# Optimization experiments

Measured on AMD Instinct MI355X. Metric: run time of the kernel, lower is better.

The kernel has to match this reference:

```python
import jax, jax.numpy as jnp
import numpy as np

B, T, D, H, L, V = 8, 1024, 1024, 16, 4, 50257
HD = D // H
DF = 4 * D
EPS = 1e-5


def _layernorm(x, w, b):
    m = jnp.mean(x, axis=-1, keepdims=True)
    v = jnp.mean((x - m) ** 2, axis=-1, keepdims=True)
    return (x - m) * jax.lax.rsqrt(v + EPS) * w + b


def setup_inputs() -> dict:
    key = jax.random.key(0)
    ks = jax.random.split(key, 17)
    s = 0.02
    n = lambda k, shape: (jax.random.normal(k, shape) * s).astype(jnp.float32)
    return {
        "idx": jax.random.randint(ks[0], (B, T), 0, V),
        "tok_emb": n(ks[1], (V, D)),
        "pos_emb": n(ks[2], (T, D)),
        "wq": n(ks[3], (L, D, D)),
        "wk": n(ks[4], (L, D, D)),
        "wv": n(ks[5], (L, D, D)),
        "w_proj": n(ks[6], (L, D, D)),
        "b_proj": jnp.zeros((L, D), jnp.float32),
        "ln1_w": jnp.ones((L, D), jnp.float32),
        "ln1_b": jnp.zeros((L, D), jnp.float32),
        "ln2_w": jnp.ones((L, D), jnp.float32),
        "ln2_b": jnp.zeros((L, D), jnp.float32),
        "w1": n(ks[7], (L, D, DF)),
        "b1": jnp.zeros((L, DF), jnp.float32),
        "w2": n(ks[8], (L, DF, D)),
        "b2": jnp.zeros((L, D), jnp.float32),
    }


def reference(idx, tok_emb, pos_emb, wq, wk, wv, w_proj, b_proj,
              ln1_w, ln1_b, ln2_w, ln2_b, w1, b1, w2, b2):
    b, t = idx.shape
    x = tok_emb[idx] + pos_emb[:t]  # [B,T,D]
    causal_mask = jnp.tril(jnp.ones((t, t), dtype=bool))  # [T,T]
    # NOTE: original scales by full embedding dim C**-0.5, not head_size
    scale = jnp.asarray(D, x.dtype) ** -0.5
    for l in range(L):
        h = _layernorm(x, ln1_w[l], ln1_b[l])
        q = (h @ wq[l]).reshape(b, t, H, HD)
        k = (h @ wk[l]).reshape(b, t, H, HD)
        v = (h @ wv[l]).reshape(b, t, H, HD)
        scores = jnp.einsum('bthd,bshd->bhts', q, k) * scale  # [B,H,T,T]
        scores = jnp.where(causal_mask, scores, -jnp.inf)
        attn = jax.nn.softmax(scores, axis=-1)
        ctx = jnp.einsum('bhts,bshd->bthd', attn, v).reshape(b, t, D)
        x = x + (ctx @ w_proj[l] + b_proj[l])
        h2 = _layernorm(x, ln2_w[l], ln2_b[l])
        ff = jax.nn.relu(h2 @ w1[l] + b1[l]) @ w2[l] + b2[l]
        x = x + ff  # fRes = 1.0 (linear_residual=True)
    return x
```

## Files before the change

### kernel.cpp

```cpp
#include <hip/hip_runtime.h>
#include <hip/hip_bf16.h>
#include <stdint.h>

typedef __hip_bfloat16 bf16;
typedef __attribute__((ext_vector_type(8))) short short8;
typedef __attribute__((ext_vector_type(4))) float f32x4;
typedef __attribute__((ext_vector_type(2))) unsigned int uint32x2;

static constexpr int TB = 8;
static constexpr int TT = 1024;
static constexpr int TD = 1024;
static constexpr int TH = 16;
static constexpr int TL = 4;
static constexpr int TDF = 4096;
static constexpr int TM = TB * TT;
static constexpr int QS = 3072;

#if __has_builtin(__builtin_amdgcn_permlane16_swap) && __has_builtin(__builtin_amdgcn_permlane32_swap)
#define USE_PERMLANE 1
#else
#define USE_PERMLANE 0
#endif

#define GLOAD16(g, l) __builtin_amdgcn_global_load_lds( \
    (const __attribute__((address_space(1))) unsigned int*)(g), \
    (__attribute__((address_space(3))) unsigned int*)(l), 16, 0, 0)

__global__ __launch_bounds__(256) void k_embed(const int* __restrict__ idx,
        const float* __restrict__ tok, const float* __restrict__ pos,
        float* __restrict__ x) {
    int row = blockIdx.x;
    int t = row & (TT - 1);
    int token = idx[row];
    int c = threadIdx.x * 4;
    float4 tv = *(const float4*)(tok + (int64_t)token * TD + c);
    float4 pv = *(const float4*)(pos + (int64_t)t * TD + c);
    *(float4*)(x + (int64_t)row * TD + c) =
        make_float4(tv.x + pv.x, tv.y + pv.y, tv.z + pv.z, tv.w + pv.w);
}

__global__ __launch_bounds__(256) void k_ln(const float* __restrict__ x,
        const float* __restrict__ w, const float* __restrict__ b,
        bf16* __restrict__ out) {
    int row = blockIdx.x;
    int tid = threadIdx.x;
    const float* xr = x + (int64_t)row * TD;
    float4 v = *(const float4*)(xr + tid * 4);
    float s  = v.x + v.y + v.z + v.w;
    float s2 = v.x*v.x + v.y*v.y + v.z*v.z + v.w*v.w;
    #pragma unroll
    for (int off = 32; off; off >>= 1) { s += __shfl_xor(s, off); s2 += __shfl_xor(s2, off); }
    __shared__ float red[8];
    int wv_ = tid >> 6, ln_ = tid & 63;
    if (ln_ == 0) { red[wv_] = s; red[4 + wv_] = s2; }
    __syncthreads();
    s  = red[0] + red[1] + red[2] + red[3];
    s2 = red[4] + red[5] + red[6] + red[7];
    float mean = s * (1.f / TD);
    float var  = s2 * (1.f / TD) - mean * mean;
    float rstd = rsqrtf(var + 1e-5f);
    float4 wv4 = *(const float4*)(w + tid * 4);
    float4 bv4 = *(const float4*)(b + tid * 4);
    bf16 t4[4];
    t4[0] = __float2bfloat16((v.x - mean) * rstd * wv4.x + bv4.x);
    t4[1] = __float2bfloat16((v.y - mean) * rstd * wv4.y + bv4.y);
    t4[2] = __float2bfloat16((v.z - mean) * rstd * wv4.z + bv4.z);
    t4[3] = __float2bfloat16((v.w - mean) * rstd * wv4.w + bv4.w);
    *(uint2*)(out + (int64_t)row * TD + tid * 4) = *(uint2*)t4;
}

__global__ __launch_bounds__(256) void k_wt(
        const float* __restrict__ wq, const float* __restrict__ wk,
        const float* __restrict__ wv, const float* __restrict__ wp,
        const float* __restrict__ w1, const float* __restrict__ w2,
        bf16* __restrict__ qkvT, bf16* __restrict__ wpT,
        bf16* __restrict__ w1T, bf16* __restrict__ w2T) {
    __shared__ bf16 tile[64 * 74];
    const int id = blockIdx.x;
    const float* src; bf16* dst; int K, N, n0, k0;
    if (id < 768) {
        int w = id >> 8, r = id & 255;
        src = (w == 0) ? wq : ((w == 1) ? wk : wv);
        dst = qkvT + (int64_t)w * 1024 * 1024;
        K = 1024; N = 1024; n0 = (r & 15) * 64; k0 = (r >> 4) * 64;
    } else if (id < 1024) {
        int r = id - 768; src = wp; dst = wpT;
        K = 1024; N = 1024; n0 = (r & 15) * 64; k0 = (r >> 4) * 64;
    } else if (id < 2048) {
        int r = id - 1024; src = w1; dst = w1T;
        K = 1024; N = 4096; n0 = (r & 63) * 64; k0 = (r >> 6) * 64;
    } else {
        int r = id - 2048; src = w2; dst = w2T;
        K = 4096; N = 1024; n0 = (r & 15) * 64; k0 = (r >> 4) * 64;
    }
    const int tid = threadIdx.x;
    #pragma unroll
    for (int i = 0; i < 16; i++) {
        int q = i * 256 + tid;
        int r = q >> 6, c = q & 63;
        tile[r * 74 + c] = __float2bfloat16(src[(int64_t)(k0 + r) * N + n0 + c]);
    }
    __syncthreads();
    #pragma unroll
    for (int i = 0; i < 16; i++) {
        int q = i * 256 + tid;
        int nr = q >> 6, kc = q & 63;
        dst[(int64_t)(n0 + nr) * K + k0 + kc] = tile[kc * 74 + nr];
    }
}

template<int EPI>
__global__ __launch_bounds__(512, 2) void k_gemm256(const bf16* __restrict__ A,
        const bf16* __restrict__ BT, const float* __restrict__ bias,
        const float* __restrict__ resid,
        float* __restrict__ outF, bf16* __restrict__ outB,
        bf16* __restrict__ vtp, int M, int N, int K) {
    extern __shared__ __align__(16) char smem[];
    const int tid = threadIdx.x;
    const int lane = tid & 63, wave = tid >> 6;
    const int wm = wave >> 2, wn = wave & 3;
    const int lr = lane & 15, lk = lane >> 4;
    const int nb = gridDim.x;
    const int sb = (blockIdx.x & 7) * (nb >> 3) + (blockIdx.x >> 3);
    const int nbn = N >> 8;
    const int bm = sb / nbn, bn = sb % nbn;
    const int64_t aBase = (int64_t)bm * 256 * K;
    const int64_t bBase = (int64_t)bn * 256 * K;
    const int NT = K >> 6;

    const int tswz = tid ^ (((tid >> 5) & 1) << 1);
    const int row0 = tswz >> 3, s0 = tswz & 7;

#define STAGE256(tt) do { \
        char* Ad_ = smem + (((tt) & 1) << 15); \
        char* Bd_ = smem + 65536 + (((tt) & 1) << 15); \
        _Pragma("unroll") \
        for (int j = 0; j < 4; j++) { \
            const int rr_ = j * 64 + row0; \
            GLOAD16(A  + aBase + (int64_t)rr_ * K + (tt) * 64 + s0 * 8, Ad_ + (j * 512 + tid) * 16); \
            GLOAD16(BT + bBase + (int64_t)rr_ * K + (tt) * 64 + s0 * 8, Bd_ + (j * 512 + tid) * 16); \
        } \
    } while (0)

    f32x4 acc[8][4] = {};
    const int lkx = lk ^ ((lr & 4) >> 1);
    const int aoff = wm * 8192 + lr * 64 + lkx * 8;
    const int boff = wn * 4096 + lr * 64 + lkx * 8;

    STAGE256(0);
    STAGE256(1);
    asm volatile("s_waitcnt vmcnt(8)" ::: "memory");
    __builtin_amdgcn_s_barrier();

    for (int t = 0; t < NT; ++t) {
        const bf16* Ab = (const bf16*)(smem + ((t & 1) << 15));
        const bf16* Bb = (const bf16*)(smem + 65536 + ((t & 1) << 15));
        short8 af[2][8], bv[2][4];
        #pragma unroll
        for (int kk = 0; kk < 2; kk++) {
            #pragma unroll
            for (int m = 0; m < 8; m++)
                af[kk][m] = *(const short8*)(Ab + aoff + m * 1024 + kk * 32);
            #pragma unroll
            for (int n = 0; n < 4; n++)
                bv[kk][n] = *(const short8*)(Bb + boff + n * 1024 + kk * 32);
        }
        asm volatile("s_waitcnt lgkmcnt(0)" ::: "memory");
        __builtin_amdgcn_sched_barrier(0);
        __builtin_amdgcn_s_barrier();
        if (t + 2 < NT) STAGE256(t + 2);
        __builtin_amdgcn_s_setprio(1);
        #pragma unroll
        for (int kk = 0; kk < 2; kk++)
            #pragma unroll
            for (int fm = 0; fm < 8; fm++)
                #pragma unroll
                for (int fn = 0; fn < 4; fn++)
                    acc[fm][fn] = __builtin_amdgcn_mfma_f32_16x16x32_bf16(
                        af[kk][fm], bv[kk][fn], acc[fm][fn], 0, 0, 0);
        __builtin_amdgcn_s_setprio(0);
        if (t + 2 < NT) {
            asm volatile("s_waitcnt vmcnt(8)" ::: "memory");
            __builtin_amdgcn_s_barrier();
        } else if (t + 1 < NT) {
            asm volatile("s_waitcnt vmcnt(0)" ::: "memory");
            __builtin_amdgcn_s_barrier();
        }
    }
#undef STAGE256

    #pragma unroll
    for (int fm = 0; fm < 8; fm++) {
        #pragma unroll
        for (int fn = 0; fn < 4; fn++) {
            const int col = bn * 256 + wn * 64 + fn * 16 + lr;
            if constexpr (EPI & 16) {
                const int trow = bm * 256 + wm * 128 + fm * 16 + lk * 4;
                if (col >= 2048) {
                    const int d = col - 2048;
                    bf16 t4[4];
                    #pragma unroll
                    for (int r = 0; r < 4; r++)
                        t4[r] = __float2bfloat16(acc[fm][fn][r]);
                    const int bb = trow >> 10, tt2 = trow & 1023;
                    *(uint2*)(vtp + ((int64_t)((bb * TH + (d >> 6)) * 64 + (d & 63)) * TT + tt2)) = *(uint2*)t4;
                } else {
                    #pragma unroll
                    for (int r = 0; r < 4; r++)
                        outB[(int64_t)(trow + r) * N + col] = __float2bfloat16(acc[fm][fn][r]);
                }
            } else {
                #pragma unroll
                for (int r = 0; r < 4; r++) {
                    const int row = bm * 256 + wm * 128 + fm * 16 + lk * 4 + r;
                    float v = acc[fm][fn][r];
                    if constexpr (EPI & 1) v += bias[col];
                    if constexpr (EPI & 2) v = fmaxf(v, 0.f);
                    if constexpr (EPI & 4) v += resid[(int64_t)row * N + col];
                    if constexpr (EPI & 8) outF[(int64_t)row * N + col] = v;
                    else outB[(int64_t)row * N + col] = __float2bfloat16(v);
                }
            }
        }
    }
}

template<int EPI>
__global__ __launch_bounds__(512, 2) void k_gemm128d(const bf16* __restrict__ A,
        const bf16* __restrict__ BT, const float* __restrict__ bias,
        const float* __restrict__ resid,
        float* __restrict__ outF, bf16* __restrict__ outB, int M, int N, int K) {
    extern __shared__ __align__(16) char smem[];
    const int tid = threadIdx.x;
    const int lane = tid & 63, wave = tid >> 6;
    const int wm = wave >> 2, wn = wave & 3;
    const int lr = lane & 15, lk = lane >> 4;
    const int nb = gridDim.x;
    const int sb = (blockIdx.x & 7) * (nb >> 3) + (blockIdx.x >> 3);
    const int nbn = N >> 7;
    const int bm = sb / nbn, bn = sb % nbn;
    const int64_t aBase = (int64_t)bm * 128 * K;
    const int64_t bBase = (int64_t)bn * 128 * K;
    const int NT = K >> 6;

    const int tswz = tid ^ (((tid >> 5) & 1) << 1);
    const int row0 = tswz >> 3, s0 = tswz & 7;

#define STAGE128D(tt) do { \
        char* Ad_ = smem + (((tt) & 1) << 14); \
        char* Bd_ = smem + 32768 + (((tt) & 1) << 14); \
        _Pragma("unroll") \
        for (int j = 0; j < 2; j++) { \
            const int rr_ = j * 64 + row0; \
            GLOAD16(A  + aBase + (int64_t)rr_ * K + (tt) * 64 + s0 * 8, Ad_ + (j * 512 + tid) * 16); \
            GLOAD16(BT + bBase + (int64_t)rr_ * K + (tt) * 64 + s0 * 8, Bd_ + (j * 512 + tid) * 16); \
        } \
    } while (0)

    f32x4 acc[4][2] = {};
    const int lkx = lk ^ ((lr & 4) >> 1);
    const int aoff = wm * 4096 + lr * 64 + lkx * 8;
    const int boff = wn * 2048 + lr * 64 + lkx * 8;

    STAGE128D(0);
    STAGE128D(1);
    asm volatile("s_waitcnt vmcnt(4)" ::: "memory");
    __builtin_amdgcn_s_barrier();

    for (int t = 0; t < NT; ++t) {
        const bf16* Ab = (const bf16*)(smem + ((t & 1) << 14));
        const bf16* Bb = (const bf16*)(smem + 32768 + ((t & 1) << 14));
        short8 af[2][4], bv[2][2];
        #pragma unroll
        for (int kk = 0; kk < 2; kk++) {
            #pragma unroll
            for (int m = 0; m < 4; m++)
                af[kk][m] = *(const short8*)(Ab + aoff + m * 1024 + kk * 32);
            #pragma unroll
            for (int n = 0; n < 2; n++)
                bv[kk][n] = *(const short8*)(Bb + boff + n * 1024 + kk * 32);
        }
        asm volatile("s_waitcnt lgkmcnt(0)" ::: "memory");
        __builtin_amdgcn_sched_barrier(0);
        __builtin_amdgcn_s_barrier();
        if (t + 2 < NT) STAGE128D(t + 2);
        __builtin_amdgcn_s_setprio(1);
        #pragma unroll
        for (int kk = 0; kk < 2; kk++)
            #pragma unroll
            for (int fm = 0; fm < 4; fm++)
                #pragma unroll
                for (int fn = 0; fn < 2; fn++)
                    acc[fm][fn] = __builtin_amdgcn_mfma_f32_16x16x32_bf16(
                        af[kk][fm], bv[kk][fn], acc[fm][fn], 0, 0, 0);
        __builtin_amdgcn_s_setprio(0);
        if (t + 2 < NT) {
            asm volatile("s_waitcnt vmcnt(4)" ::: "memory");
            __builtin_amdgcn_s_barrier();
        } else if (t + 1 < NT) {
            asm volatile("s_waitcnt vmcnt(0)" ::: "memory");
            __builtin_amdgcn_s_barrier();
        }
    }
#undef STAGE128D

    #pragma unroll
    for (int fm = 0; fm < 4; fm++) {
        #pragma unroll
        for (int fn = 0; fn < 2; fn++) {
            const int col = bn * 128 + wn * 32 + fn * 16 + lr;
            #pragma unroll
            for (int r = 0; r < 4; r++) {
                const int row = bm * 128 + wm * 64 + fm * 16 + lk * 4 + r;
                float v = acc[fm][fn][r];
                if constexpr (EPI & 1) v += bias[col];
                if constexpr (EPI & 2) v = fmaxf(v, 0.f);
                if constexpr (EPI & 4) v += resid[(int64_t)row * N + col];
                if constexpr (EPI & 8) outF[(int64_t)row * N + col] = v;
                else outB[(int64_t)row * N + col] = __float2bfloat16(v);
            }
        }
    }
}

#if USE_PERMLANE
__device__ __forceinline__ float redmax16(float v) {
    uint32x2 s = __builtin_amdgcn_permlane16_swap(
        __float_as_uint(v), __float_as_uint(v), false, false);
    return fmaxf(__uint_as_float(s[0]), __uint_as_float(s[1]));
}
__device__ __forceinline__ float redmax32(float v) {
    uint32x2 s = __builtin_amdgcn_permlane32_swap(
        __float_as_uint(v), __float_as_uint(v), false, false);
    return fmaxf(__uint_as_float(s[0]), __uint_as_float(s[1]));
}
#endif

__device__ __forceinline__ void attn_tile(int k0, int qg, int nk,
        short8 qf0, short8 qf1,
        short8 kf00, short8 kf01, short8 kf10, short8 kf11,
        const short8 (&vf)[4], f32x4 (&ctx)[4], float& mrun, float& lrun,
        int c, int g, float scale2) {
    f32x4 st0 = {}, st1 = {};
    __builtin_amdgcn_s_setprio(1);
    st0 = __builtin_amdgcn_mfma_f32_16x16x32_bf16(kf00, qf0, st0, 0, 0, 0);
    st0 = __builtin_amdgcn_mfma_f32_16x16x32_bf16(kf01, qf1, st0, 0, 0, 0);
    const bool h2 = (k0 + 16 < nk);
    if (h2) {
        st1 = __builtin_amdgcn_mfma_f32_16x16x32_bf16(kf10, qf0, st1, 0, 0, 0);
        st1 = __builtin_amdgcn_mfma_f32_16x16x32_bf16(kf11, qf1, st1, 0, 0, 0);
    }
    __builtin_amdgcn_s_setprio(0);
    float sv[8];
    #pragma unroll
    for (int r = 0; r < 4; r++) {
        int kg = k0 + 4 * g + r;
        sv[r] = (kg <= qg) ? st0[r] * scale2 : -INFINITY;
    }
    #pragma unroll
    for (int r = 0; r < 4; r++) {
        int kg = k0 + 16 + 4 * g + r;
        sv[4 + r] = (h2 && kg <= qg) ? st1[r] * scale2 : -INFINITY;
    }
    float bm = sv[0];
    #pragma unroll
    for (int i = 1; i < 8; i++) bm = fmaxf(bm, sv[i]);
#if USE_PERMLANE
    bm = redmax32(redmax16(bm));
#else
    bm = fmaxf(bm, __shfl_xor(bm, 16));
    bm = fmaxf(bm, __shfl_xor(bm, 32));
#endif
    if (__any(bm > mrun + 11.5416f)) {
        const float mnew = fmaxf(mrun, bm);
        const float facc = exp2f(mrun - mnew);
        lrun *= facc;
        #pragma unroll
        for (int dt = 0; dt < 4; dt++) ctx[dt] *= facc;
        mrun = mnew;
    }
    float p[8], psum = 0.f;
    #pragma unroll
    for (int i = 0; i < 8; i++) { p[i] = exp2f(sv[i] - mrun); psum += p[i]; }
    lrun += psum;

    auto pk = [](float a, float b2) -> uint32_t {
        uint16_t lo = __hip_bfloat16_raw(__float2bfloat16(a)).x;
        uint16_t hi = __hip_bfloat16_raw(__float2bfloat16(b2)).x;
        return (uint32_t)lo | ((uint32_t)hi << 16);
    };
    uint32_t w00 = pk(p[0], p[1]), w01 = pk(p[2], p[3]);
    uint32_t w10 = pk(p[4], p[5]), w11 = pk(p[6], p[7]);
    union { uint32_t u[4]; short8 v; } pa;
#if USE_PERMLANE
    uint32x2 sA = __builtin_amdgcn_permlane32_swap(w00, w10, false, false);
    uint32x2 sA2 = __builtin_amdgcn_permlane16_swap(sA[0], sA[1], false, false);
    uint32x2 sB = __builtin_amdgcn_permlane32_swap(w01, w11, false, false);
    uint32x2 sB2 = __builtin_amdgcn_permlane16_swap(sB[0], sB[1], false, false);
    pa.u[0] = sA2[0]; pa.u[2] = sA2[1];
    pa.u[1] = sB2[0]; pa.u[3] = sB2[1];
#else
    const int srcA = c + ((g & 1) << 5);
    const int srcB = srcA + 16;
    uint32_t x0 = (uint32_t)__shfl((int)w00, srcA);
    uint32_t x1 = (uint32_t)__shfl((int)w01, srcA);
    uint32_t x2 = (uint32_t)__shfl((int)w00, srcB);
    uint32_t x3 = (uint32_t)__shfl((int)w01, srcB);
    uint32_t y0 = (uint32_t)__shfl((int)w10, srcA);
    uint32_t y1 = (uint32_t)__shfl((int)w11, srcA);
    uint32_t y2 = (uint32_t)__shfl((int)w10, srcB);
    uint32_t y3 = (uint32_t)__shfl((int)w11, srcB);
    const bool hi2 = (g >= 2);
    pa.u[0] = hi2 ? y0 : x0; pa.u[1] = hi2 ? y1 : x1;
    pa.u[2] = hi2 ? y2 : x2; pa.u[3] = hi2 ? y3 : x3;
#endif

    __builtin_amdgcn_s_setprio(1);
    #pragma unroll
    for (int dt = 0; dt < 4; dt++)
        ctx[dt] = __builtin_amdgcn_mfma_f32_16x16x32_bf16(vf[dt], pa.v, ctx[dt], 0, 0, 0);
    __builtin_amdgcn_s_setprio(0);
}

__global__ __launch_bounds__(256) void k_attn5(const bf16* __restrict__ qkv,
        const bf16* __restrict__ Vt, bf16* __restrict__ O) {
    const int lane = threadIdx.x & 63;
    const int wave = threadIdx.x >> 6;
    int bid = (blockIdx.x & 7) * 128 + (blockIdx.x >> 3);
    const int wid = bid * 4 + wave;
    const int qp = wid & 31, h = (wid >> 5) & 15, b = wid >> 9;
    const int q0A = qp * 16, q0B = (63 - qp) * 16;
    const int c = lane & 15, g = lane >> 4;
    const int qgA = q0A + c, qgB = q0B + c;
    const float scale2 = 1.4426950408889634f / 32.0f;

    const bf16* Qp = qkv;
    const bf16* Kp = qkv + 1024;

    const bf16* qrowA = Qp + ((int64_t)(b * TT + q0A + c)) * QS + h * 64 + g * 8;
    short8 qA0 = *(const short8*)(qrowA);
    short8 qA1 = *(const short8*)(qrowA + 32);
    const bf16* qrowB = Qp + ((int64_t)(b * TT + q0B + c)) * QS + h * 64 + g * 8;
    short8 qB0 = *(const short8*)(qrowB);
    short8 qB1 = *(const short8*)(qrowB + 32);

    f32x4 ctxA[4] = {}, ctxB[4] = {};
    float mA = -INFINITY, lA = 0.f, mB = -INFINITY, lB = 0.f;

    const bf16* kbase = Kp + ((int64_t)b * TT) * QS + h * 64 + c * QS + g * 8;
    const bf16* vbase = Vt + ((int64_t)(b * TH + h) * 64) * TT + (int64_t)c * TT + g * 8;

    const int nkA = q0A + 16, nkB = q0B + 16;

    short8 ka0, ka1, ka2, ka3, va0, va1, va2, va3;
    short8 kb0, kb1, kb2, kb3, vb0, vb1, vb2, vb3;

#define LOADK(K0, NK, F0, F1, F2, F3) do { \
        const bf16* kp_ = kbase + (int64_t)(K0) * QS; \
        F0 = *(const short8*)(kp_); \
        F1 = *(const short8*)(kp_ + 32); \
        if ((K0) + 16 < (NK)) { \
            F2 = *(const short8*)(kp_ + 16 * QS); \
            F3 = *(const short8*)(kp_ + 16 * QS + 32); \
        } else { F2 = (short8){}; F3 = (short8){}; } \
    } while (0)
#define LOADV(K0, V0, V1, V2, V3) do { \
        const bf16* vp_ = vbase + (K0); \
        V0 = *(const short8*)(vp_); \
        V1 = *(const short8*)(vp_ + 16 * TT); \
        V2 = *(const short8*)(vp_ + 32 * TT); \
        V3 = *(const short8*)(vp_ + 48 * TT); \
    } while (0)

    LOADK(0, nkB, ka0, ka1, ka2, ka3);
    LOADV(0, va0, va1, va2, va3);

    for (int k0 = 0; k0 < nkB; k0 += 64) {
        const int kn1 = k0 + 32;
        if (kn1 < nkB) {
            LOADK(kn1, nkB, kb0, kb1, kb2, kb3);
            LOADV(kn1, vb0, vb1, vb2, vb3);
        }
        {
            const short8 vfa[4] = {va0, va1, va2, va3};
            attn_tile(k0, qgB, nkB, qB0, qB1, ka0, ka1, ka2, ka3, vfa,
                      ctxB, mB, lB, c, g, scale2);
            if (k0 < nkA)
                attn_tile(k0, qgA, nkA, qA0, qA1, ka0, ka1, ka2, ka3, vfa,
                          ctxA, mA, lA, c, g, scale2);
        }
        if (kn1 < nkB) {
            const int kn2 = k0 + 64;
            if (kn2 < nkB) {
                LOADK(kn2, nkB, ka0, ka1, ka2, ka3);
                LOADV(kn2, va0, va1, va2, va3);
            }
            const short8 vfb[4] = {vb0, vb1, vb2, vb3};
            attn_tile(kn1, qgB, nkB, qB0, qB1, kb0, kb1, kb2, kb3, vfb,
                      ctxB, mB, lB, c, g, scale2);
            if (kn1 < nkA)
                attn_tile(kn1, qgA, nkA, qA0, qA1, kb0, kb1, kb2, kb3, vfb,
                          ctxA, mA, lA, c, g, scale2);
        }
    }
#undef LOADK
#undef LOADV

    lA += __shfl_xor(lA, 16); lA += __shfl_xor(lA, 32);
    lB += __shfl_xor(lB, 16); lB += __shfl_xor(lB, 32);

    const float invA = 1.0f / lA, invB = 1.0f / lB;
    bf16* orowA = O + ((int64_t)(b * TT + q0A + c)) * TD + h * 64 + g * 4;
    bf16* orowB = O + ((int64_t)(b * TT + q0B + c)) * TD + h * 64 + g * 4;
    #pragma unroll
    for (int dt = 0; dt < 4; dt++) {
        bf16 t4[4];
        #pragma unroll
        for (int r = 0; r < 4; r++) t4[r] = __float2bfloat16(ctxA[dt][r] * invA);
        *(uint2*)(orowA + dt * 16) = *(uint2*)t4;
        #pragma unroll
        for (int r = 0; r < 4; r++) t4[r] = __float2bfloat16(ctxB[dt][r] * invB);
        *(uint2*)(orowB + dt * 16) = *(uint2*)t4;
    }
}

extern "C" void kernel_launch(void* const* d_in, const int* in_sizes, int n_in,
                              void* d_out, int out_size, void* d_ws, size_t ws_size,
                              hipStream_t stream) {
    const int*   idx  = (const int*)  d_in[0];
    const float* tok  = (const float*)d_in[1];
    const float* pos  = (const float*)d_in[2];
    const float* wq   = (const float*)d_in[3];
    const float* wk   = (const float*)d_in[4];
    const float* wv   = (const float*)d_in[5];
    const float* wp   = (const float*)d_in[6];
    const float* bp   = (const float*)d_in[7];
    const float* ln1w = (const float*)d_in[8];
    const float* ln1b = (const float*)d_in[9];
    const float* ln2w = (const float*)d_in[10];
    const float* ln2b = (const float*)d_in[11];
    const float* w1   = (const float*)d_in[12];
    const float* b1   = (const float*)d_in[13];
    const float* w2   = (const float*)d_in[14];
    const float* b2   = (const float*)d_in[15];
    float* x = (float*)d_out;

    char* ws = (char*)d_ws;
    size_t off = 0;
    auto alloc = [&](size_t bytes) {
        char* p = ws + off; off += (bytes + 255) & ~(size_t)255; return p;
    };
    bf16* h    = (bf16*)alloc((size_t)TM * TD * 2);
    bf16* qkv  = (bf16*)alloc((size_t)TM * QS * 2);
    bf16* ctx  = (bf16*)alloc((size_t)TM * TD * 2);
    bf16* ffa  = (bf16*)alloc((size_t)TM * TDF * 2);
    bf16* qkvT = (bf16*)alloc((size_t)3 * TD * TD * 2);
    bf16* wpT  = (bf16*)alloc((size_t)TD * TD * 2);
    bf16* w1T  = (bf16*)alloc((size_t)TD * TDF * 2);
    bf16* w2T  = (bf16*)alloc((size_t)TD * TDF * 2);
    bf16* vt   = (bf16*)ffa;

    hipFuncSetAttribute((const void*)k_gemm256<16>,
        hipFuncAttributeMaxDynamicSharedMemorySize, 131072);
    hipFuncSetAttribute((const void*)k_gemm256<3>,
        hipFuncAttributeMaxDynamicSharedMemorySize, 131072);
    hipFuncSetAttribute((const void*)k_gemm128d<13>,
        hipFuncAttributeMaxDynamicSharedMemorySize, 65536);

    k_embed<<<TM, 256, 0, stream>>>(idx, tok, pos, x);

    const int gQKV = (TM / 256) * (QS / 256);
    const int gF1  = (TM / 256) * (TDF / 256);
    const int gN1K = (TM / 128) * (TD / 128);

    for (int l = 0; l < TL; l++) {
        k_wt<<<3072, 256, 0, stream>>>(
            wq + (int64_t)l * TD * TD, wk + (int64_t)l * TD * TD,
            wv + (int64_t)l * TD * TD, wp + (int64_t)l * TD * TD,
            w1 + (int64_t)l * TD * TDF, w2 + (int64_t)l * TDF * TD,
            qkvT, wpT, w1T, w2T);

        k_ln<<<TM, 256, 0, stream>>>(x, ln1w + l * TD, ln1b + l * TD, h);
        k_gemm256<16><<<gQKV, 512, 131072, stream>>>(h, qkvT, nullptr, nullptr, nullptr, qkv, vt, TM, QS, TD);
        k_attn5<<<1024, 256, 0, stream>>>(qkv, vt, ctx);
        k_gemm128d<13><<<gN1K, 512, 65536, stream>>>(ctx, wpT, bp + l * TD, x, x, nullptr, TM, TD, TD);
        k_ln<<<TM, 256, 0, stream>>>(x, ln2w + l * TD, ln2b + l * TD, h);
        k_gemm256<3><<<gF1, 512, 131072, stream>>>(h, w1T, b1 + l * TDF, nullptr, nullptr, ffa, nullptr, TM, TDF, TD);
        k_gemm128d<13><<<gN1K, 512, 65536, stream>>>(ffa, w2T, b2 + l * TD, x, x, nullptr, TM, TD, TDF);
    }
    (void)in_sizes; (void)n_in; (void)out_size; (void)ws_size;
}
```

Before: 1.623 ms.

## Share K/V tiles across eight waves via double-buffered LDS in attention

The attention kernel now runs 512-thread blocks of eight waves that all belong to the same (batch, head). K and V tiles of 64 keys are staged cooperatively into an XOR-swizzled, double-buffered LDS buffer with global_load_lds, replacing per-wave direct global loads. This is meant to cut redundant global/L2 traffic for K and V across waves. In exchange it adds a block-wide barrier per tile and makes every wave iterate up to the block's longest causal range.

```diff
diff --git a/kernel.cpp b/kernel.cpp
--- a/kernel.cpp
+++ b/kernel.cpp
@@ -422,21 +422,21 @@
     __builtin_amdgcn_s_setprio(0);
 }
 
-__global__ __launch_bounds__(256) void k_attn5(const bf16* __restrict__ qkv,
+__global__ __launch_bounds__(512) void k_attn6(const bf16* __restrict__ qkv,
         const bf16* __restrict__ Vt, bf16* __restrict__ O) {
-    const int lane = threadIdx.x & 63;
-    const int wave = threadIdx.x >> 6;
-    int bid = (blockIdx.x & 7) * 128 + (blockIdx.x >> 3);
-    const int wid = bid * 4 + wave;
-    const int qp = wid & 31, h = (wid >> 5) & 15, b = wid >> 9;
+    __shared__ __align__(16) bf16 kv[2][2][64 * 64];
+    const int tid = threadIdx.x;
+    const int lane = tid & 63;
+    const int wave = tid >> 6;
+    const int sbid = (blockIdx.x & 7) * 64 + (blockIdx.x >> 3);
+    const int qp = ((sbid * 8) & 31) + wave;
+    const int h = (sbid >> 2) & 15, b = sbid >> 6;
     const int q0A = qp * 16, q0B = (63 - qp) * 16;
     const int c = lane & 15, g = lane >> 4;
     const int qgA = q0A + c, qgB = q0B + c;
     const float scale2 = 1.4426950408889634f / 32.0f;
 
     const bf16* Qp = qkv;
-    const bf16* Kp = qkv + 1024;
-
     const bf16* qrowA = Qp + ((int64_t)(b * TT + q0A + c)) * QS + h * 64 + g * 8;
     short8 qA0 = *(const short8*)(qrowA);
     short8 qA1 = *(const short8*)(qrowA + 32);
@@ -447,64 +447,58 @@
     f32x4 ctxA[4] = {}, ctxB[4] = {};
     float mA = -INFINITY, lA = 0.f, mB = -INFINITY, lB = 0.f;
 
-    const bf16* kbase = Kp + ((int64_t)b * TT) * QS + h * 64 + c * QS + g * 8;
-    const bf16* vbase = Vt + ((int64_t)(b * TH + h) * 64) * TT + (int64_t)c * TT + g * 8;
+    const bf16* kg = qkv + 1024 + ((int64_t)b * TT) * QS + h * 64;
+    const bf16* vg = Vt + ((int64_t)(b * TH + h) * 64) * TT;
 
     const int nkA = q0A + 16, nkB = q0B + 16;
-
-    short8 ka0, ka1, ka2, ka3, va0, va1, va2, va3;
-    short8 kb0, kb1, kb2, kb3, vb0, vb1, vb2, vb3;
-
-#define LOADK(K0, NK, F0, F1, F2, F3) do { \
-        const bf16* kp_ = kbase + (int64_t)(K0) * QS; \
-        F0 = *(const short8*)(kp_); \
-        F1 = *(const short8*)(kp_ + 32); \
-        if ((K0) + 16 < (NK)) { \
-            F2 = *(const short8*)(kp_ + 16 * QS); \
-            F3 = *(const short8*)(kp_ + 16 * QS + 32); \
-        } else { F2 = (short8){}; F3 = (short8){}; } \
+    const int nkMax = (63 - ((sbid * 8) & 31)) * 16 + 16;
+
+    const int row0 = tid >> 3, s0 = tid & 7, sx = (s0 ^ (row0 & 7)) * 8;
+
+#define STAGEKV(bi, K0) do { \
+        GLOAD16(kg + (int64_t)((K0) + row0) * QS + sx, &kv[bi][0][tid * 8]); \
+        GLOAD16(vg + (int64_t)row0 * TT + (K0) + sx,   &kv[bi][1][tid * 8]); \
     } while (0)
-#define LOADV(K0, V0, V1, V2, V3) do { \
-        const bf16* vp_ = vbase + (K0); \
-        V0 = *(const short8*)(vp_); \
-        V1 = *(const short8*)(vp_ + 16 * TT); \
-        V2 = *(const short8*)(vp_ + 32 * TT); \
-        V3 = *(const short8*)(vp_ + 48 * TT); \
-    } while (0)
-
-    LOADK(0, nkB, ka0, ka1, ka2, ka3);
-    LOADV(0, va0, va1, va2, va3);
-
-    for (int k0 = 0; k0 < nkB; k0 += 64) {
-        const int kn1 = k0 + 32;
-        if (kn1 < nkB) {
-            LOADK(kn1, nkB, kb0, kb1, kb2, kb3);
-            LOADV(kn1, vb0, vb1, vb2, vb3);
-        }
-        {
-            const short8 vfa[4] = {va0, va1, va2, va3};
-            attn_tile(k0, qgB, nkB, qB0, qB1, ka0, ka1, ka2, ka3, vfa,
-                      ctxB, mB, lB, c, g, scale2);
-            if (k0 < nkA)
-                attn_tile(k0, qgA, nkA, qA0, qA1, ka0, ka1, ka2, ka3, vfa,
-                          ctxA, mA, lA, c, g, scale2);
-        }
-        if (kn1 < nkB) {
-            const int kn2 = k0 + 64;
-            if (kn2 < nkB) {
-                LOADK(kn2, nkB, ka0, ka1, ka2, ka3);
-                LOADV(kn2, va0, va1, va2, va3);
+
+    auto kread = [&](int bi, int row, int ch) -> short8 {
+        return *(const short8*)&kv[bi][0][row * 64 + ((ch ^ (row & 7)) * 8)];
+    };
+    auto vread = [&](int bi, int row, int ch) -> short8 {
+        return *(const short8*)&kv[bi][1][row * 64 + ((ch ^ (row & 7)) * 8)];
+    };
+
+    STAGEKV(0, 0);
+    asm volatile("s_waitcnt vmcnt(0)" ::: "memory");
+    __syncthreads();
+
+    int bi = 0;
+    for (int k0 = 0; k0 < nkMax; k0 += 64) {
+        if (k0 + 64 < nkMax) STAGEKV(bi ^ 1, k0 + 64);
+        #pragma unroll
+        for (int sb2 = 0; sb2 < 2; sb2++) {
+            const int kl = sb2 * 32;
+            const int ks = k0 + kl;
+            if (ks < nkB) {
+                short8 kf00 = kread(bi, kl + c, g);
+                short8 kf01 = kread(bi, kl + c, g + 4);
+                short8 kf10 = kread(bi, kl + 16 + c, g);
+                short8 kf11 = kread(bi, kl + 16 + c, g + 4);
+                short8 vf[4];
+                #pragma unroll
+                for (int dt = 0; dt < 4; dt++)
+                    vf[dt] = vread(bi, dt * 16 + c, (sb2 << 2) + g);
+                attn_tile(ks, qgB, nkB, qB0, qB1, kf00, kf01, kf10, kf11, vf,
+                          ctxB, mB, lB, c, g, scale2);
+                if (ks < nkA)
+                    attn_tile(ks, qgA, nkA, qA0, qA1, kf00, kf01, kf10, kf11, vf,
+                              ctxA, mA, lA, c, g, scale2);
             }
-            const short8 vfb[4] = {vb0, vb1, vb2, vb3};
-            attn_tile(kn1, qgB, nkB, qB0, qB1, kb0, kb1, kb2, kb3, vfb,
-                      ctxB, mB, lB, c, g, scale2);
-            if (kn1 < nkA)
-                attn_tile(kn1, qgA, nkA, qA0, qA1, kb0, kb1, kb2, kb3, vfb,
-                          ctxA, mA, lA, c, g, scale2);
-        }
-    }
-#undef LOADK
-#undef LOADV
+        }
+        asm volatile("s_waitcnt vmcnt(0)" ::: "memory");
+        __syncthreads();
+        bi ^= 1;
+    }
+#undef STAGEKV
 
     lA += __shfl_xor(lA, 16); lA += __shfl_xor(lA, 32);
     lB += __shfl_xor(lB, 16); lB += __shfl_xor(lB, 32);
@@ -582,7 +576,7 @@
 
         k_ln<<<TM, 256, 0, stream>>>(x, ln1w + l * TD, ln1b + l * TD, h);
         k_gemm256<16><<<gQKV, 512, 131072, stream>>>(h, qkvT, nullptr, nullptr, nullptr, qkv, vt, TM, QS, TD);
-        k_attn5<<<1024, 256, 0, stream>>>(qkv, vt, ctx);
+        k_attn6<<<512, 512, 0, stream>>>(qkv, vt, ctx);
         k_gemm128d<13><<<gN1K, 512, 65536, stream>>>(ctx, wpT, bp + l * TD, x, x, nullptr, TM, TD, TD);
         k_ln<<<TM, 256, 0, stream>>>(x, ln2w + l * TD, ln2b + l * TD, h);
         k_gemm256<3><<<gF1, 512, 131072, stream>>>(h, w1T, b1 + l * TDF, nullptr, nullptr, ffa, nullptr, TM, TDF, TD);
```

Result: faster. 1.361 ms (-16.1%).
